# Kernel optimization log

Measured on AMD Instinct MI355X. Metric: run time of the kernel, lower is better.

The kernel has to match this reference:

```python
import jax, jax.numpy as jnp
import numpy as np

# SqueezeSeg CRF config
NUM_CLASS = 4
SIZE_Z, SIZE_A = 3, 5            # LCN_HEIGHT, LCN_WIDTH
B, H, W = 16, 64, 512            # batch, zenith, azimuth
RCRF_ITER = 3
BI_FILTER_COEF = 0.1
ANG_FILTER_COEF = 0.02
ANG_THETA_A = 0.9
BILATERAL_THETA_A = 0.9
K = SIZE_Z * SIZE_A              # 15 -> 14 neighbors (center excluded)

# neighbor offsets of the 3x5 condensing kernel, center excluded
OFFSETS = [(dz, da) for dz in range(SIZE_Z) for da in range(SIZE_A)
           if not (dz == SIZE_Z // 2 and da == SIZE_A // 2)]

def _gauss_weights(theta_sq):
    # angular_filter_kernel: Gaussian of squared spatial offset, center zeroed
    g = [np.exp(-((dz - SIZE_Z // 2) ** 2 + (da - SIZE_A // 2) ** 2) / (2.0 * theta_sq))
         for dz, da in OFFSETS]
    return jnp.asarray(np.array(g, dtype=np.float32))

def gather_neighbors(x):
    # x: [B,C,H,W] -> [B,C,K-1,H,W]; zero-padded 'same' neighborhood gather
    pz, pa = SIZE_Z // 2, SIZE_A // 2
    xp = jnp.pad(x, ((0, 0), (0, 0), (pz, pz), (pa, pa)))
    return jnp.stack([xp[:, :, dz:dz + H, da:da + W] for dz, da in OFFSETS], axis=2)

def setup_inputs() -> dict:
    key = jax.random.key(0)
    k1, k2, k3 = jax.random.split(key, 3)
    x = jax.random.normal(k1, (B, NUM_CLASS, H, W), dtype=jnp.float32)
    bilateral_filters = jax.random.uniform(k2, (B, 1, K - 1, H, W), dtype=jnp.float32)
    lidar_mask = (jax.random.uniform(k3, (B, 1, H, W)) > 0.5).astype(jnp.float32)
    return {"x": x, "bilateral_filters": bilateral_filters, "lidar_mask": lidar_mask}

def reference(x, bilateral_filters, lidar_mask):
    g_ang = _gauss_weights(ANG_THETA_A ** 2)
    g_bi = _gauss_weights(BILATERAL_THETA_A ** 2)
    compat = jnp.ones((NUM_CLASS, NUM_CLASS), jnp.float32) - jnp.eye(NUM_CLASS, dtype=jnp.float32)
    ang_compat = compat * ANG_FILTER_COEF   # [out_class, in_class] 1x1 conv
    bi_compat = compat * BI_FILTER_COEF

    for _ in range(RCRF_ITER):
        unary = jax.nn.softmax(x, axis=1)                     # softmax over class dim
        nb = gather_neighbors(unary)                          # [B,C,14,H,W]
        # depthwise angular filters = Gaussian-weighted neighbor sums
        ang = jnp.einsum('k,bckhw->bchw', g_ang, nb)
        bi_ang = jnp.einsum('k,bckhw->bchw', g_bi, nb)
        # condensing conv on masked unary, weighted by per-pixel bilateral filters
        nb_m = gather_neighbors(unary * lidar_mask)           # [B,C,14,H,W]
        condensed = jnp.sum(nb_m * bilateral_filters, axis=2) # [B,C,H,W]
        bi = condensed * lidar_mask * bi_ang
        # 1x1 compatibility transforms
        ang2 = jnp.einsum('oc,bchw->bohw', ang_compat, ang)
        bi2 = jnp.einsum('oc,bchw->bohw', bi_compat, bi)
        x = unary + ang2 + bi2
    return x
```

## Files before the change

kernel.cpp:

```cpp
#include <hip/hip_runtime.h>


#define NCLASS 4
#define HH 64
#define WW 512
#define BB 16
#define TH 4
#define TW 64
#define HALO_H (TH + 2)
#define HALO_W (TW + 4)
#define PLANE (HH * WW)

#define G1 0.53940412f
#define G2 0.29095687f
#define G4 0.08466190f
#define G5 0.04566227f

__global__ __launch_bounds__(256, 6) void crf_iter(
    const float* __restrict__ xin,
    const float* __restrict__ filt,
    const float* __restrict__ mask,
    float* __restrict__ xout)
{
    __shared__ float u_lds[NCLASS][HALO_H][HALO_W];
    __shared__ float m_lds[HALO_H][HALO_W];

    const int b  = blockIdx.z;
    const int h0 = blockIdx.y * TH;
    const int w0 = blockIdx.x * TW;
    const int tid = threadIdx.x;

    for (int idx = tid; idx < HALO_H * HALO_W; idx += 256) {
        const int lr = idx / HALO_W;
        const int lc = idx - lr * HALO_W;
        const int gh = h0 + lr - 1;
        const int gw = w0 + lc - 2;
        if (gh >= 0 && gh < HH && gw >= 0 && gw < WW) {
            const int base = (b * NCLASS * HH + gh) * WW + gw;
            const float v0 = xin[base + 0 * PLANE];
            const float v1 = xin[base + 1 * PLANE];
            const float v2 = xin[base + 2 * PLANE];
            const float v3 = xin[base + 3 * PLANE];
            const float mx = fmaxf(fmaxf(v0, v1), fmaxf(v2, v3));
            const float e0 = expf(v0 - mx);
            const float e1 = expf(v1 - mx);
            const float e2 = expf(v2 - mx);
            const float e3 = expf(v3 - mx);
            const float inv = 1.0f / (e0 + e1 + e2 + e3);
            u_lds[0][lr][lc] = e0 * inv;
            u_lds[1][lr][lc] = e1 * inv;
            u_lds[2][lr][lc] = e2 * inv;
            u_lds[3][lr][lc] = e3 * inv;
            m_lds[lr][lc] = mask[(b * HH + gh) * WW + gw];
        } else {
            u_lds[0][lr][lc] = 0.0f;
            u_lds[1][lr][lc] = 0.0f;
            u_lds[2][lr][lc] = 0.0f;
            u_lds[3][lr][lc] = 0.0f;
            m_lds[lr][lc] = 0.0f;
        }
    }
    __syncthreads();

    const int DZ[14]   = {0,0,0,0,0, 1,1,1,1, 2,2,2,2,2};
    const int DA[14]   = {0,1,2,3,4, 0,1,3,4, 0,1,2,3,4};
    const float GW[14] = {G5,G2,G1,G2,G5, G4,G1,G1,G4, G5,G2,G1,G2,G5};

    const int r  = tid >> 6;
    const int cc = tid & 63;
    const int gh = h0 + r;
    const int gw = w0 + cc;

    float ang[NCLASS]  = {0.f, 0.f, 0.f, 0.f};
    float cond[NCLASS] = {0.f, 0.f, 0.f, 0.f};
    const float mc = m_lds[r + 1][cc + 2];
    const int fpix = (b * 14 * HH + gh) * WW + gw;

#pragma unroll
    for (int k = 0; k < 14; ++k) {
        const float f  = filt[fpix + k * PLANE];
        const int lr = r + DZ[k];
        const int lc = cc + DA[k];
        const float mn = m_lds[lr][lc];
        const float fm = f * mn;
        const float gk = GW[k];
#pragma unroll
        for (int c = 0; c < NCLASS; ++c) {
            const float un = u_lds[c][lr][lc];
            ang[c]  = fmaf(gk, un, ang[c]);
            cond[c] = fmaf(fm, un, cond[c]);
        }
    }

    float bi[NCLASS];
    float sa = 0.f, sb = 0.f;
#pragma unroll
    for (int c = 0; c < NCLASS; ++c) {
        bi[c] = cond[c] * mc * ang[c];
        sa += ang[c];
        sb += bi[c];
    }

    const int obase = (b * NCLASS * HH + gh) * WW + gw;
#pragma unroll
    for (int c = 0; c < NCLASS; ++c) {
        const float uc = u_lds[c][r + 1][cc + 2];
        xout[obase + c * PLANE] =
            uc + 0.02f * (sa - ang[c]) + 0.1f * (sb - bi[c]);
    }
}

extern "C" void kernel_launch(void* const* d_in, const int* in_sizes, int n_in,
                              void* d_out, int out_size, void* d_ws, size_t ws_size,
                              hipStream_t stream) {
    const float* x    = (const float*)d_in[0];
    const float* filt = (const float*)d_in[1];
    const float* msk  = (const float*)d_in[2];
    float* out = (float*)d_out;
    float* ws0 = (float*)d_ws;

    dim3 grid(WW / TW, HH / TH, BB);
    dim3 block(256);

    crf_iter<<<grid, block, 0, stream>>>(x,   filt, msk, out);
    crf_iter<<<grid, block, 0, stream>>>(out, filt, msk, ws0);
    crf_iter<<<grid, block, 0, stream>>>(ws0, filt, msk, out);
}
```

Before: 102.5 us.

## Fuse three CRF iterations into one kernel with halo recompute

Replaces three launches with a single kernel that loads a 3-row/6-column halo, then recomputes shrinking regions for each iteration, keeping softmaxed state in LDS as float4. This removes intermediate global writes/reads of x and two launches, at the cost of redundant halo computation and repeated filter reads. Also doubles tile height, switches to fast __expf, and packs classes into float4 LDS entries.

Result: faster. 98.66 us (-3.7%).

```diff
diff --git a/kernel.cpp b/kernel.cpp
--- a/kernel.cpp
+++ b/kernel.cpp
@@ -5,10 +5,10 @@
 #define HH 64
 #define WW 512
 #define BB 16
-#define TH 4
+#define TH 8
 #define TW 64
-#define HALO_H (TH + 2)
-#define HALO_W (TW + 4)
+#define UR (TH + 6)
+#define UC (TW + 12)
 #define PLANE (HH * WW)
 
 #define G1 0.53940412f
@@ -16,98 +16,143 @@
 #define G4 0.08466190f
 #define G5 0.04566227f
 
-__global__ __launch_bounds__(256, 6) void crf_iter(
+#define TAPS                                                                 \
+    const int   DZ[14] = {-1,-1,-1,-1,-1,  0, 0, 0, 0,  1, 1, 1, 1, 1};      \
+    const int   DA[14] = {-2,-1, 0, 1, 2, -2,-1, 1, 2, -2,-1, 0, 1, 2};      \
+    const float GW[14] = {G5,G2,G1,G2,G5, G4,G1,G1,G4, G5,G2,G1,G2,G5};
+
+template <int MR, int MC, bool FINAL>
+__device__ __forceinline__ void crf_step(
+    float4 (*__restrict__ u_lds)[UC], const float (*__restrict__ m_lds)[UC],
+    const float* __restrict__ filt, float* __restrict__ dst,
+    int b, int h0, int w0, int tid)
+{
+    constexpr int RH = TH + 2 * MR;
+    constexpr int RW = TW + 2 * MC;
+    constexpr int NS = (RH * RW + 255) / 256;
+    TAPS
+
+    float4 xnew[NS];
+
+#pragma unroll
+    for (int j = 0; j < NS; ++j) {
+        const int s = tid + 256 * j;
+        float4 r = make_float4(0.f, 0.f, 0.f, 0.f);
+        if (s < RH * RW) {
+            const int lr = s / RW;
+            const int lc = s - lr * RW;
+            const int gh = h0 + lr - MR;
+            const int gw = w0 + lc - MC;
+            const int ur = lr + (3 - MR);
+            const int uc = lc + (6 - MC);
+            if (gh >= 0 && gh < HH && gw >= 0 && gw < WW) {
+                float a0 = 0.f, a1 = 0.f, a2 = 0.f, a3 = 0.f;
+                float c0 = 0.f, c1 = 0.f, c2 = 0.f, c3 = 0.f;
+                const float mcen = m_lds[ur][uc];
+                const float* fp = filt + ((size_t)b * 14 * HH + gh) * WW + gw;
+#pragma unroll
+                for (int k = 0; k < 14; ++k) {
+                    const float  f  = fp[(size_t)k * PLANE];
+                    const float  mn = m_lds[ur + DZ[k]][uc + DA[k]];
+                    const float4 u  = u_lds[ur + DZ[k]][uc + DA[k]];
+                    const float  fm = f * mn;
+                    const float  gk = GW[k];
+                    a0 = fmaf(gk, u.x, a0);  c0 = fmaf(fm, u.x, c0);
+                    a1 = fmaf(gk, u.y, a1);  c1 = fmaf(fm, u.y, c1);
+                    a2 = fmaf(gk, u.z, a2);  c2 = fmaf(fm, u.z, c2);
+                    a3 = fmaf(gk, u.w, a3);  c3 = fmaf(fm, u.w, c3);
+                }
+                const float b0 = c0 * mcen * a0;
+                const float b1 = c1 * mcen * a1;
+                const float b2 = c2 * mcen * a2;
+                const float b3 = c3 * mcen * a3;
+                const float sa = a0 + a1 + a2 + a3;
+                const float sb = b0 + b1 + b2 + b3;
+                const float4 ucen = u_lds[ur][uc];
+                r.x = ucen.x + 0.02f * (sa - a0) + 0.1f * (sb - b0);
+                r.y = ucen.y + 0.02f * (sa - a1) + 0.1f * (sb - b1);
+                r.z = ucen.z + 0.02f * (sa - a2) + 0.1f * (sb - b2);
+                r.w = ucen.w + 0.02f * (sa - a3) + 0.1f * (sb - b3);
+                if (!FINAL) {
+                    const float mx  = fmaxf(fmaxf(r.x, r.y), fmaxf(r.z, r.w));
+                    const float e0  = __expf(r.x - mx);
+                    const float e1  = __expf(r.y - mx);
+                    const float e2  = __expf(r.z - mx);
+                    const float e3  = __expf(r.w - mx);
+                    const float inv = 1.0f / (e0 + e1 + e2 + e3);
+                    r = make_float4(e0 * inv, e1 * inv, e2 * inv, e3 * inv);
+                }
+            }
+            if (FINAL) {
+                float* o = dst + ((size_t)b * NCLASS * HH + gh) * WW + gw;
+                o[0]         = r.x;
+                o[PLANE]     = r.y;
+                o[2 * PLANE] = r.z;
+                o[3 * PLANE] = r.w;
+            }
+        }
+        if (!FINAL) xnew[j] = r;
+    }
+
+    if (!FINAL) {
+        __syncthreads();
+#pragma unroll
+        for (int j = 0; j < NS; ++j) {
+            const int s = tid + 256 * j;
+            if (s < RH * RW) {
+                const int lr = s / RW;
+                const int lc = s - lr * RW;
+                u_lds[lr + (3 - MR)][lc + (6 - MC)] = xnew[j];
+            }
+        }
+        __syncthreads();
+    }
+}
+
+__global__ __launch_bounds__(256, 4) void crf_fused(
     const float* __restrict__ xin,
     const float* __restrict__ filt,
     const float* __restrict__ mask,
     float* __restrict__ xout)
 {
-    __shared__ float u_lds[NCLASS][HALO_H][HALO_W];
-    __shared__ float m_lds[HALO_H][HALO_W];
+    __shared__ float4 u_lds[UR][UC];
+    __shared__ float  m_lds[UR][UC];
 
-    const int b  = blockIdx.z;
-    const int h0 = blockIdx.y * TH;
-    const int w0 = blockIdx.x * TW;
+    const int b   = blockIdx.z;
+    const int h0  = blockIdx.y * TH;
+    const int w0  = blockIdx.x * TW;
     const int tid = threadIdx.x;
 
-    for (int idx = tid; idx < HALO_H * HALO_W; idx += 256) {
-        const int lr = idx / HALO_W;
-        const int lc = idx - lr * HALO_W;
-        const int gh = h0 + lr - 1;
-        const int gw = w0 + lc - 2;
+    for (int idx = tid; idx < UR * UC; idx += 256) {
+        const int lr = idx / UC;
+        const int lc = idx - lr * UC;
+        const int gh = h0 + lr - 3;
+        const int gw = w0 + lc - 6;
+        float4 u = make_float4(0.f, 0.f, 0.f, 0.f);
+        float  m = 0.f;
         if (gh >= 0 && gh < HH && gw >= 0 && gw < WW) {
-            const int base = (b * NCLASS * HH + gh) * WW + gw;
-            const float v0 = xin[base + 0 * PLANE];
-            const float v1 = xin[base + 1 * PLANE];
-            const float v2 = xin[base + 2 * PLANE];
-            const float v3 = xin[base + 3 * PLANE];
+            const float* px = xin + ((size_t)b * NCLASS * HH + gh) * WW + gw;
+            const float v0 = px[0];
+            const float v1 = px[PLANE];
+            const float v2 = px[2 * PLANE];
+            const float v3 = px[3 * PLANE];
             const float mx = fmaxf(fmaxf(v0, v1), fmaxf(v2, v3));
-            const float e0 = expf(v0 - mx);
-            const float e1 = expf(v1 - mx);
-            const float e2 = expf(v2 - mx);
-            const float e3 = expf(v3 - mx);
+            const float e0 = __expf(v0 - mx);
+            const float e1 = __expf(v1 - mx);
+            const float e2 = __expf(v2 - mx);
+            const float e3 = __expf(v3 - mx);
             const float inv = 1.0f / (e0 + e1 + e2 + e3);
-            u_lds[0][lr][lc] = e0 * inv;
-            u_lds[1][lr][lc] = e1 * inv;
-            u_lds[2][lr][lc] = e2 * inv;
-            u_lds[3][lr][lc] = e3 * inv;
-            m_lds[lr][lc] = mask[(b * HH + gh) * WW + gw];
-        } else {
-            u_lds[0][lr][lc] = 0.0f;
-            u_lds[1][lr][lc] = 0.0f;
-            u_lds[2][lr][lc] = 0.0f;
-            u_lds[3][lr][lc] = 0.0f;
-            m_lds[lr][lc] = 0.0f;
+            u = make_float4(e0 * inv, e1 * inv, e2 * inv, e3 * inv);
+            m = mask[((size_t)b * HH + gh) * WW + gw];
         }
+        u_lds[lr][lc] = u;
+        m_lds[lr][lc] = m;
     }
     __syncthreads();
 
-    const int DZ[14]   = {0,0,0,0,0, 1,1,1,1, 2,2,2,2,2};
-    const int DA[14]   = {0,1,2,3,4, 0,1,3,4, 0,1,2,3,4};
-    const float GW[14] = {G5,G2,G1,G2,G5, G4,G1,G1,G4, G5,G2,G1,G2,G5};
-
-    const int r  = tid >> 6;
-    const int cc = tid & 63;
-    const int gh = h0 + r;
-    const int gw = w0 + cc;
-
-    float ang[NCLASS]  = {0.f, 0.f, 0.f, 0.f};
-    float cond[NCLASS] = {0.f, 0.f, 0.f, 0.f};
-    const float mc = m_lds[r + 1][cc + 2];
-    const int fpix = (b * 14 * HH + gh) * WW + gw;
-
-#pragma unroll
-    for (int k = 0; k < 14; ++k) {
-        const float f  = filt[fpix + k * PLANE];
-        const int lr = r + DZ[k];
-        const int lc = cc + DA[k];
-        const float mn = m_lds[lr][lc];
-        const float fm = f * mn;
-        const float gk = GW[k];
-#pragma unroll
-        for (int c = 0; c < NCLASS; ++c) {
-            const float un = u_lds[c][lr][lc];
-            ang[c]  = fmaf(gk, un, ang[c]);
-            cond[c] = fmaf(fm, un, cond[c]);
-        }
-    }
-
-    float bi[NCLASS];
-    float sa = 0.f, sb = 0.f;
-#pragma unroll
-    for (int c = 0; c < NCLASS; ++c) {
-        bi[c] = cond[c] * mc * ang[c];
-        sa += ang[c];
-        sb += bi[c];
-    }
-
-    const int obase = (b * NCLASS * HH + gh) * WW + gw;
-#pragma unroll
-    for (int c = 0; c < NCLASS; ++c) {
-        const float uc = u_lds[c][r + 1][cc + 2];
-        xout[obase + c * PLANE] =
-            uc + 0.02f * (sa - ang[c]) + 0.1f * (sb - bi[c]);
-    }
+    crf_step<2, 4, false>(u_lds, m_lds, filt, xout, b, h0, w0, tid);
+    crf_step<1, 2, false>(u_lds, m_lds, filt, xout, b, h0, w0, tid);
+    crf_step<0, 0, true >(u_lds, m_lds, filt, xout, b, h0, w0, tid);
 }
 
 extern "C" void kernel_launch(void* const* d_in, const int* in_sizes, int n_in,
@@ -117,12 +162,9 @@
     const float* filt = (const float*)d_in[1];
     const float* msk  = (const float*)d_in[2];
     float* out = (float*)d_out;
-    float* ws0 = (float*)d_ws;
+    (void)d_ws; (void)ws_size;
 
     dim3 grid(WW / TW, HH / TH, BB);
     dim3 block(256);
-
-    crf_iter<<<grid, block, 0, stream>>>(x,   filt, msk, out);
-    crf_iter<<<grid, block, 0, stream>>>(out, filt, msk, ws0);
-    crf_iter<<<grid, block, 0, stream>>>(ws0, filt, msk, out);
+    crf_fused<<<grid, block, 0, stream>>>(x, filt, msk, out);
 }
```
